# Optimization experiments

Hardware: AMD Instinct MI355X
Metric: run time of the kernel (lower is better)

Reference implementation:

```python
import jax, jax.numpy as jnp
import numpy as np

N = 100000       # nodes
E = 1600000      # edges (avg degree 16)
F_IN = 128       # ogb_feature_dim
HID = 128        # hidden_dim
C = 40           # num_class


def setup_inputs() -> dict:
    key = jax.random.key(0)
    ks = jax.random.split(key, 6)
    w = lambda k, sh: jax.random.normal(k, sh, jnp.float32) * 0.05
    return {
        "x": jax.random.normal(ks[0], (N, F_IN), jnp.float32),
        "edge_index": jax.random.randint(ks[1], (2, E), 0, N),
        "W1": w(ks[2], (F_IN, HID)), "b1": jnp.zeros((HID,), jnp.float32),
        "W2": w(ks[3], (HID, HID)), "b2": jnp.zeros((HID,), jnp.float32),
        "W3": w(ks[4], (HID, C)),  "b3": jnp.zeros((C,), jnp.float32),
    }


def _gcn_conv(h, row, col, deg_inv_sqrt, W, b, num_nodes):
    # PyG GCNConv: x' = D^{-1/2} (A + I) D^{-1/2} (x W) + b
    h = h @ W                                   # [N, out]
    norm = deg_inv_sqrt[row] * deg_inv_sqrt[col]  # [E+N]
    msg = h[row] * norm[:, None]                # gather + scale (irregular)
    out = jax.ops.segment_sum(msg, col, num_segments=num_nodes)  # scatter-add
    return out + b


def reference(x, edge_index, W1, b1, W2, b2, W3, b3):
    num_nodes = x.shape[0]
    loops = jnp.arange(num_nodes, dtype=edge_index.dtype)
    row = jnp.concatenate([edge_index[0], loops])  # add self-loops
    col = jnp.concatenate([edge_index[1], loops])
    deg = jax.ops.segment_sum(jnp.ones_like(col, jnp.float32), col,
                              num_segments=num_nodes)
    deg_inv_sqrt = jax.lax.rsqrt(jnp.maximum(deg, 1e-12))  # deg>=1 (self-loops)

    h = _gcn_conv(x, row, col, deg_inv_sqrt, W1, b1, num_nodes)
    h = jax.nn.relu(h)  # dropout is identity in eval mode
    h = _gcn_conv(h, row, col, deg_inv_sqrt, W2, b2, num_nodes)
    h = jax.nn.relu(h)
    h = _gcn_conv(h, row, col, deg_inv_sqrt, W3, b3, num_nodes)
    return jax.nn.log_softmax(h, axis=1)
```

## Files before the change

kernel.cpp:

```cpp
#include <hip/hip_runtime.h>
#include <hip/hip_bf16.h>
#include <math.h>


__device__ inline float bfu(unsigned short s) {
    return __uint_as_float((unsigned)s << 16);
}
__device__ inline float bf16lo(unsigned u) { return __uint_as_float(u << 16); }
__device__ inline float bf16hi(unsigned u) { return __uint_as_float(u & 0xFFFF0000u); }
__device__ inline unsigned packbf2(float a, float b) {
    __hip_bfloat16 x = __float2bfloat16(a), y = __float2bfloat16(b);
    unsigned short ux = *(unsigned short*)&x, uy = *(unsigned short*)&y;
    return (unsigned)ux | ((unsigned)uy << 16);
}
__device__ inline unsigned short bf1(float a) {
    __hip_bfloat16 x = __float2bfloat16(a);
    return *(unsigned short*)&x;
}

__global__ __launch_bounds__(256) void k_bhist(const int* __restrict__ col, int E,
                                               int NB, int* __restrict__ bhist) {
    __shared__ int h[512];
    for (int j = threadIdx.x; j < 512; j += 256) h[j] = 0;
    __syncthreads();
    int chunk = (E + gridDim.x - 1) / gridDim.x;
    int lo = blockIdx.x * chunk;
    int hi = min(lo + chunk, E);
    for (int i = lo + threadIdx.x; i < hi; i += 256)
        atomicAdd(&h[col[i] >> 8], 1);
    __syncthreads();
    for (int j = threadIdx.x; j < NB; j += 256) {
        int v = h[j];
        if (v) atomicAdd(&bhist[j], v);
    }
}

__global__ __launch_bounds__(512) void k_bscan(const int* __restrict__ bhist,
                                               int NB, int E,
                                               int* __restrict__ bbase,
                                               int* __restrict__ bcur) {
    __shared__ int sm[512];
    int t = threadIdx.x;
    int v = (t < NB) ? bhist[t] : 0;
    sm[t] = v;
    __syncthreads();
    for (int off = 1; off < 512; off <<= 1) {
        int u = (t >= off) ? sm[t - off] : 0;
        __syncthreads();
        sm[t] += u;
        __syncthreads();
    }
    if (t < NB) {
        int ex = sm[t] - v;
        bbase[t] = ex;
        bcur[t] = ex;
    }
    if (t == 0) bbase[NB] = E;
}

__global__ __launch_bounds__(256) void k_bin2(const int* __restrict__ row,
                                              const int* __restrict__ col, int E,
                                              int* __restrict__ bcur,
                                              unsigned* __restrict__ binned) {
    __shared__ int h[512];
    __shared__ int base[512];
    int t = threadIdx.x;
    for (int j = t; j < 512; j += 256) h[j] = 0;
    __syncthreads();
    int chunk = (E + gridDim.x - 1) / gridDim.x;
    int lo = blockIdx.x * chunk;
    int hi = min(lo + chunk, E);
    for (int i = lo + t; i < hi; i += 256)
        atomicAdd(&h[col[i] >> 8], 1);
    __syncthreads();
    for (int j = t; j < 512; j += 256) {
        int c = h[j];
        base[j] = c ? atomicAdd(&bcur[j], c) : 0;
    }
    __syncthreads();
    for (int i = lo + t; i < hi; i += 256) {
        int r = row[i], c = col[i];
        int p = atomicAdd(&base[c >> 8], 1);
        binned[p] = (unsigned)r | ((unsigned)(c & 255) << 24);
    }
}

__global__ __launch_bounds__(256) void k_cntB(const unsigned* __restrict__ binned,
                                              const int* __restrict__ bbase,
                                              int N, int* __restrict__ cnt) {
    int b = blockIdx.x, t = threadIdx.x;
    __shared__ int sc[256];
    sc[t] = 0;
    __syncthreads();
    int lo = bbase[b], hi = bbase[b + 1];
    for (int i = lo + t; i < hi; i += 256)
        atomicAdd(&sc[binned[i] >> 24], 1);
    __syncthreads();
    int node = b * 256 + t;
    if (node < N) cnt[node] = sc[t];
}

__global__ __launch_bounds__(256) void k_bsum(const int* __restrict__ cnt, int N,
                                              int* __restrict__ bsum) {
    int t = threadIdx.x;
    int base = blockIdx.x * 1024 + t * 4;
    int s = 0;
    if (base + 3 < N) {
        int4 v = *(const int4*)(cnt + base);
        s = v.x + v.y + v.z + v.w;
    } else {
        for (int j = 0; j < 4; ++j)
            if (base + j < N) s += cnt[base + j];
    }
#pragma unroll
    for (int off = 32; off; off >>= 1) s += __shfl_xor(s, off);
    __shared__ int ws[4];
    int lane = t & 63, w = t >> 6;
    if (lane == 0) ws[w] = s;
    __syncthreads();
    if (t == 0) bsum[blockIdx.x] = ws[0] + ws[1] + ws[2] + ws[3];
}

__global__ __launch_bounds__(128) void k_sbsum(int* __restrict__ bsum, int B) {
    __shared__ int sm[128];
    int t = threadIdx.x;
    int v = (t < B) ? bsum[t] : 0;
    sm[t] = v;
    __syncthreads();
    for (int off = 1; off < 128; off <<= 1) {
        int u = (t >= off) ? sm[t - off] : 0;
        __syncthreads();
        sm[t] += u;
        __syncthreads();
    }
    if (t < B) bsum[t] = sm[t] - v;
}

__global__ __launch_bounds__(256) void k_wptr(const int* __restrict__ cnt,
                                              const int* __restrict__ bsum, int N,
                                              int* __restrict__ ptr,
                                              float* __restrict__ dis) {
    int t = threadIdx.x;
    int base = blockIdx.x * 1024 + t * 4;
    int c[4];
    int s = 0;
    if (base + 3 < N) {
        int4 v = *(const int4*)(cnt + base);
        c[0] = v.x; c[1] = v.y; c[2] = v.z; c[3] = v.w;
        s = v.x + v.y + v.z + v.w;
    } else {
#pragma unroll
        for (int j = 0; j < 4; ++j) {
            c[j] = (base + j < N) ? cnt[base + j] : 0;
            s += c[j];
        }
    }
    int lane = t & 63, w = t >> 6;
    int incl = s;
#pragma unroll
    for (int off = 1; off < 64; off <<= 1) {
        int u = __shfl_up(incl, off);
        if (lane >= off) incl += u;
    }
    __shared__ int wsum[4];
    if (lane == 63) wsum[w] = incl;
    __syncthreads();
    int run = bsum[blockIdx.x] + (incl - s);
    for (int j = 0; j < w; ++j) run += wsum[j];
#pragma unroll
    for (int j = 0; j < 4; ++j) {
        int i = base + j;
        if (i < N) {
            ptr[i] = run;
            dis[i] = rsqrtf((float)(c[j] + 1));
            run += c[j];
        }
    }
}

__global__ __launch_bounds__(256) void k_fill2(const unsigned* __restrict__ binned,
                                               const int* __restrict__ bbase,
                                               const int* __restrict__ ptr, int N,
                                               int* __restrict__ esrc) {
    int b = blockIdx.x, t = threadIdx.x;
    __shared__ int lc[256];
    int node = b * 256 + t;
    lc[t] = (node < N) ? ptr[node] : 0;
    __syncthreads();
    int lo = bbase[b], hi = bbase[b + 1];
    for (int i = lo + t; i < hi; i += 256) {
        unsigned e = binned[i];
        int p = atomicAdd(&lc[e >> 24], 1);
        esrc[p] = (int)(e & 0xFFFFFFu);
    }
}

__global__ __launch_bounds__(256) void k_gemm128_f32(const float* __restrict__ X,
                                                     const float* __restrict__ W,
                                                     unsigned short* __restrict__ Y,
                                                     int M) {
    __shared__ float wsm[64 * 128];
    __shared__ float xs[64 * 68];
    int t = threadIdx.x;
    int row0 = blockIdx.x * 64;
    int cg = t & 15, rg = t >> 4;
    float acc[4][8];
#pragma unroll
    for (int a = 0; a < 4; ++a)
#pragma unroll
        for (int b = 0; b < 8; ++b) acc[a][b] = 0.f;

    for (int kp = 0; kp < 2; ++kp) {
        const float4* W4 = (const float4*)W;
        float4* wd = (float4*)wsm;
#pragma unroll
        for (int i = 0; i < 8; ++i) {
            int idx = t + i * 256;
            wd[idx] = W4[kp * 2048 + idx];
        }
        const float4* X4 = (const float4*)X;
#pragma unroll
        for (int i = 0; i < 4; ++i) {
            int idx = t + i * 256;
            int r = idx >> 4, c4 = idx & 15;
            float4 v = {0.f, 0.f, 0.f, 0.f};
            if (row0 + r < M) v = X4[(size_t)(row0 + r) * 32 + kp * 16 + c4];
            float* dst = &xs[r * 68 + c4 * 4];
            dst[0] = v.x; dst[1] = v.y; dst[2] = v.z; dst[3] = v.w;
        }
        __syncthreads();
#pragma unroll 4
        for (int k = 0; k < 64; ++k) {
            float a0 = xs[(rg * 4 + 0) * 68 + k];
            float a1 = xs[(rg * 4 + 1) * 68 + k];
            float a2 = xs[(rg * 4 + 2) * 68 + k];
            float a3 = xs[(rg * 4 + 3) * 68 + k];
            const float* wr = &wsm[k * 128 + cg * 8];
            float4 w0 = *(const float4*)wr;
            float4 w1 = *(const float4*)(wr + 4);
            float wv[8] = {w0.x, w0.y, w0.z, w0.w, w1.x, w1.y, w1.z, w1.w};
#pragma unroll
            for (int b = 0; b < 8; ++b) {
                acc[0][b] = fmaf(a0, wv[b], acc[0][b]);
                acc[1][b] = fmaf(a1, wv[b], acc[1][b]);
                acc[2][b] = fmaf(a2, wv[b], acc[2][b]);
                acc[3][b] = fmaf(a3, wv[b], acc[3][b]);
            }
        }
        __syncthreads();
    }
#pragma unroll
    for (int a = 0; a < 4; ++a) {
        int r = row0 + rg * 4 + a;
        if (r < M) {
            uint4 o;
            o.x = packbf2(acc[a][0], acc[a][1]);
            o.y = packbf2(acc[a][2], acc[a][3]);
            o.z = packbf2(acc[a][4], acc[a][5]);
            o.w = packbf2(acc[a][6], acc[a][7]);
            *(uint4*)&Y[(size_t)r * 128 + cg * 8] = o;
        }
    }
}

__global__ __launch_bounds__(256) void k_gemm128_bf16(const unsigned short* __restrict__ X,
                                                      const float* __restrict__ W,
                                                      unsigned short* __restrict__ Y,
                                                      int M) {
    __shared__ float wsm[64 * 128];
    __shared__ float xs[64 * 68];
    int t = threadIdx.x;
    int row0 = blockIdx.x * 64;
    int cg = t & 15, rg = t >> 4;
    float acc[4][8];
#pragma unroll
    for (int a = 0; a < 4; ++a)
#pragma unroll
        for (int b = 0; b < 8; ++b) acc[a][b] = 0.f;

    for (int kp = 0; kp < 2; ++kp) {
        const float4* W4 = (const float4*)W;
        float4* wd = (float4*)wsm;
#pragma unroll
        for (int i = 0; i < 8; ++i) {
            int idx = t + i * 256;
            wd[idx] = W4[kp * 2048 + idx];
        }
        const ushort4* X4 = (const ushort4*)X;
#pragma unroll
        for (int i = 0; i < 4; ++i) {
            int idx = t + i * 256;
            int r = idx >> 4, c4 = idx & 15;
            float v0 = 0.f, v1 = 0.f, v2 = 0.f, v3 = 0.f;
            if (row0 + r < M) {
                ushort4 v = X4[(size_t)(row0 + r) * 32 + kp * 16 + c4];
                v0 = bfu(v.x); v1 = bfu(v.y); v2 = bfu(v.z); v3 = bfu(v.w);
            }
            float* dst = &xs[r * 68 + c4 * 4];
            dst[0] = v0; dst[1] = v1; dst[2] = v2; dst[3] = v3;
        }
        __syncthreads();
#pragma unroll 4
        for (int k = 0; k < 64; ++k) {
            float a0 = xs[(rg * 4 + 0) * 68 + k];
            float a1 = xs[(rg * 4 + 1) * 68 + k];
            float a2 = xs[(rg * 4 + 2) * 68 + k];
            float a3 = xs[(rg * 4 + 3) * 68 + k];
            const float* wr = &wsm[k * 128 + cg * 8];
            float4 w0 = *(const float4*)wr;
            float4 w1 = *(const float4*)(wr + 4);
            float wv[8] = {w0.x, w0.y, w0.z, w0.w, w1.x, w1.y, w1.z, w1.w};
#pragma unroll
            for (int b = 0; b < 8; ++b) {
                acc[0][b] = fmaf(a0, wv[b], acc[0][b]);
                acc[1][b] = fmaf(a1, wv[b], acc[1][b]);
                acc[2][b] = fmaf(a2, wv[b], acc[2][b]);
                acc[3][b] = fmaf(a3, wv[b], acc[3][b]);
            }
        }
        __syncthreads();
    }
#pragma unroll
    for (int a = 0; a < 4; ++a) {
        int r = row0 + rg * 4 + a;
        if (r < M) {
            uint4 o;
            o.x = packbf2(acc[a][0], acc[a][1]);
            o.y = packbf2(acc[a][2], acc[a][3]);
            o.z = packbf2(acc[a][4], acc[a][5]);
            o.w = packbf2(acc[a][6], acc[a][7]);
            *(uint4*)&Y[(size_t)r * 128 + cg * 8] = o;
        }
    }
}

__global__ __launch_bounds__(320) void k_gemm40(const unsigned short* __restrict__ X,
                                                const float* __restrict__ W,
                                                float* __restrict__ Y, int M) {
    __shared__ float wsm[128 * 40];
    __shared__ float xs[64 * 133];
    int t = threadIdx.x;
    int row0 = blockIdx.x * 64;
    for (int idx = t; idx < 128 * 40; idx += 320) wsm[idx] = W[idx];
    const ushort4* X4 = (const ushort4*)X;
    for (int idx = t; idx < 2048; idx += 320) {
        int r = idx >> 5, c4 = idx & 31;
        float v0 = 0.f, v1 = 0.f, v2 = 0.f, v3 = 0.f;
        if (row0 + r < M) {
            ushort4 v = X4[(size_t)(row0 + r) * 32 + c4];
            v0 = bfu(v.x); v1 = bfu(v.y); v2 = bfu(v.z); v3 = bfu(v.w);
        }
        float* dst = &xs[r * 133 + c4 * 4];
        dst[0] = v0; dst[1] = v1; dst[2] = v2; dst[3] = v3;
    }
    __syncthreads();
    int lane = t & 63, cg = t >> 6;
    float acc[8];
#pragma unroll
    for (int b = 0; b < 8; ++b) acc[b] = 0.f;
#pragma unroll 4
    for (int k = 0; k < 128; ++k) {
        float a = xs[lane * 133 + k];
        const float* wr = &wsm[k * 40 + cg * 8];
        float4 w0 = *(const float4*)wr;
        float4 w1 = *(const float4*)(wr + 4);
        acc[0] = fmaf(a, w0.x, acc[0]); acc[1] = fmaf(a, w0.y, acc[1]);
        acc[2] = fmaf(a, w0.z, acc[2]); acc[3] = fmaf(a, w0.w, acc[3]);
        acc[4] = fmaf(a, w1.x, acc[4]); acc[5] = fmaf(a, w1.y, acc[5]);
        acc[6] = fmaf(a, w1.z, acc[6]); acc[7] = fmaf(a, w1.w, acc[7]);
    }
    int r = row0 + lane;
    if (r < M) {
        float4* dst = (float4*)&Y[(size_t)r * 40 + cg * 8];
        float4 o0 = {acc[0], acc[1], acc[2], acc[3]};
        float4 o1 = {acc[4], acc[5], acc[6], acc[7]};
        dst[0] = o0;
        dst[1] = o1;
    }
}

__global__ __launch_bounds__(256) void k_agg128(const unsigned short* __restrict__ h,
                                                const float* __restrict__ dis,
                                                const int* __restrict__ ptr,
                                                const int* __restrict__ cnt,
                                                const int* __restrict__ esrc,
                                                const float* __restrict__ bias,
                                                unsigned short* __restrict__ out,
                                                int relu, int N) {
    int node = blockIdx.x * 4 + (threadIdx.x >> 6);
    if (node >= N) return;
    int lane = threadIdx.x & 63;
    float di = dis[node];
    const unsigned* h32 = (const unsigned*)h;
    unsigned su = h32[(size_t)node * 64 + lane];
    float w = di * di;
    float ax = bf16lo(su) * w, ay = bf16hi(su) * w;
    int start = ptr[node], c = cnt[node];
    for (int base = 0; base < c; base += 64) {
        int m = min(64, c - base);
        int e = 0;
        float dsl = 0.f;
        if (lane < m) {
            e = esrc[start + base + lane];
            dsl = dis[e];
        }
        int j = 0;
        for (; j + 2 <= m; j += 2) {
            int sA = __shfl(e, j), sB = __shfl(e, j + 1);
            float scA = __shfl(dsl, j) * di;
            float scB = __shfl(dsl, j + 1) * di;
            unsigned uA = h32[(size_t)sA * 64 + lane];
            unsigned uB = h32[(size_t)sB * 64 + lane];
            ax = fmaf(bf16lo(uA), scA, ax); ay = fmaf(bf16hi(uA), scA, ay);
            ax = fmaf(bf16lo(uB), scB, ax); ay = fmaf(bf16hi(uB), scB, ay);
        }
        if (j < m) {
            int sA = __shfl(e, j);
            float scA = __shfl(dsl, j) * di;
            unsigned uA = h32[(size_t)sA * 64 + lane];
            ax = fmaf(bf16lo(uA), scA, ax); ay = fmaf(bf16hi(uA), scA, ay);
        }
    }
    float2 b = ((const float2*)bias)[lane];
    ax += b.x; ay += b.y;
    if (relu) { ax = fmaxf(ax, 0.f); ay = fmaxf(ay, 0.f); }
    ((unsigned*)out)[(size_t)node * 64 + lane] = packbf2(ax, ay);
}

__global__ __launch_bounds__(256) void k_agg40(const float* __restrict__ h,
                                               const float* __restrict__ dis,
                                               const int* __restrict__ ptr,
                                               const int* __restrict__ cnt,
                                               const int* __restrict__ esrc,
                                               const float* __restrict__ bias,
                                               float* __restrict__ out, int N) {
    int node = blockIdx.x * 4 + (threadIdx.x >> 6);
    if (node >= N) return;
    int lane = threadIdx.x & 63;
    float di = dis[node];
    float acc = 0.f;
    if (lane < 40) acc = h[(size_t)node * 40 + lane] * di * di;
    int start = ptr[node], c = cnt[node];
    for (int base = 0; base < c; base += 64) {
        int m = min(64, c - base);
        int e = 0;
        float dsl = 0.f;
        if (lane < m) {
            e = esrc[start + base + lane];
            dsl = dis[e];
        }
        for (int j = 0; j < m; ++j) {
            int s = __shfl(e, j);
            float sc = __shfl(dsl, j) * di;
            if (lane < 40) acc = fmaf(h[(size_t)s * 40 + lane], sc, acc);
        }
    }
    if (lane < 40) out[(size_t)node * 40 + lane] = acc + bias[lane];
}

__global__ __launch_bounds__(256) void k_lsm(const float* __restrict__ in,
                                             float* __restrict__ out, int N) {
    int rowi = blockIdx.x * 4 + (threadIdx.x >> 6);
    if (rowi >= N) return;
    int lane = threadIdx.x & 63;
    float v = (lane < 40) ? in[(size_t)rowi * 40 + lane] : -INFINITY;
    float m = v;
#pragma unroll
    for (int o = 32; o; o >>= 1) m = fmaxf(m, __shfl_xor(m, o));
    float ex = (lane < 40) ? expf(v - m) : 0.f;
    float s = ex;
#pragma unroll
    for (int o = 32; o; o >>= 1) s += __shfl_xor(s, o);
    if (lane < 40) out[(size_t)rowi * 40 + lane] = v - m - logf(s);
}

extern "C" void kernel_launch(void* const* d_in, const int* in_sizes, int n_in,
                              void* d_out, int out_size, void* d_ws, size_t ws_size,
                              hipStream_t stream) {
    const float* x  = (const float*)d_in[0];
    const int*   ei = (const int*)d_in[1];
    const float* W1 = (const float*)d_in[2];
    const float* b1 = (const float*)d_in[3];
    const float* W2 = (const float*)d_in[4];
    const float* b2 = (const float*)d_in[5];
    const float* W3 = (const float*)d_in[6];
    const float* b3 = (const float*)d_in[7];
    int N = in_sizes[0] / 128;
    int E = in_sizes[1] / 2;
    const int* row = ei;
    const int* col = ei + E;
    int NB = (N + 255) >> 8;

    char* ws = (char*)d_ws;
    size_t off = 0;
    auto alloc = [&](size_t bytes) {
        void* p = ws + off;
        off += (bytes + 255) & ~(size_t)255;
        return p;
    };
    unsigned short* hA = (unsigned short*)alloc((size_t)N * 128 * 2);
    unsigned short* hB = (unsigned short*)alloc((size_t)N * 128 * 2);
    float* t3    = (float*)alloc((size_t)N * 40 * 4);
    float* t3b   = (float*)alloc((size_t)N * 40 * 4);
    int*   esrc  = (int*)alloc((size_t)E * 4);
    int*   cptr  = (int*)alloc((size_t)N * 4);
    int*   cnt   = (int*)alloc((size_t)N * 4);
    float* dis   = (float*)alloc((size_t)N * 4);
    int*   bsum  = (int*)alloc(256 * 4);
    int*   bhist = (int*)alloc(512 * 4);
    int*   bbase = (int*)alloc(513 * 4);
    int*   bcur  = (int*)alloc(512 * 4);
    unsigned* binned = (unsigned*)hB;

    hipMemsetAsync(bhist, 0, 512 * 4, stream);
    k_bhist<<<256, 256, 0, stream>>>(col, E, NB, bhist);
    k_bscan<<<1, 512, 0, stream>>>(bhist, NB, E, bbase, bcur);
    k_bin2<<<256, 256, 0, stream>>>(row, col, E, bcur, binned);
    k_cntB<<<NB, 256, 0, stream>>>(binned, bbase, N, cnt);
    int B = (N + 1023) / 1024;
    k_bsum<<<B, 256, 0, stream>>>(cnt, N, bsum);
    k_sbsum<<<1, 128, 0, stream>>>(bsum, B);
    k_wptr<<<B, 256, 0, stream>>>(cnt, bsum, N, cptr, dis);
    k_fill2<<<NB, 256, 0, stream>>>(binned, bbase, cptr, N, esrc);

    int gb = (N + 63) / 64;
    int ab = (N + 3) / 4;
    k_gemm128_f32<<<gb, 256, 0, stream>>>(x, W1, hA, N);
    k_agg128<<<ab, 256, 0, stream>>>(hA, dis, cptr, cnt, esrc, b1, hB, 1, N);
    k_gemm128_bf16<<<gb, 256, 0, stream>>>(hB, W2, hA, N);
    k_agg128<<<ab, 256, 0, stream>>>(hA, dis, cptr, cnt, esrc, b2, hB, 1, N);
    k_gemm40<<<gb, 320, 0, stream>>>(hB, W3, t3, N);
    k_agg40<<<ab, 256, 0, stream>>>(t3, dis, cptr, cnt, esrc, b3, t3b, N);
    k_lsm<<<ab, 256, 0, stream>>>(t3b, (float*)d_out, N);
}
```

Baseline: 577.5 us.

## Reorder last GCN layer to aggregate before GEMM and fuse bias with log-softmax

After: 546.9 us. -5.3%, faster.

```diff
diff --git a/kernel.cpp b/kernel.cpp
--- a/kernel.cpp
+++ b/kernel.cpp
@@ -12,10 +12,6 @@
     __hip_bfloat16 x = __float2bfloat16(a), y = __float2bfloat16(b);
     unsigned short ux = *(unsigned short*)&x, uy = *(unsigned short*)&y;
     return (unsigned)ux | ((unsigned)uy << 16);
-}
-__device__ inline unsigned short bf1(float a) {
-    __hip_bfloat16 x = __float2bfloat16(a);
-    return *(unsigned short*)&x;
 }
 
 __global__ __launch_bounds__(256) void k_bhist(const int* __restrict__ col, int E,
@@ -334,11 +330,14 @@
     }
 }
 
-__global__ __launch_bounds__(320) void k_gemm40(const unsigned short* __restrict__ X,
-                                                const float* __restrict__ W,
-                                                float* __restrict__ Y, int M) {
+__global__ __launch_bounds__(320) void k_gemm40f(const unsigned short* __restrict__ X,
+                                                 const float* __restrict__ W,
+                                                 const float* __restrict__ bias,
+                                                 float* __restrict__ out, int M) {
     __shared__ float wsm[128 * 40];
     __shared__ float xs[64 * 133];
+    __shared__ float osm[64 * 40];
+    __shared__ float rm[64], rls[64];
     int t = threadIdx.x;
     int row0 = blockIdx.x * 64;
     for (int idx = t; idx < 128 * 40; idx += 320) wsm[idx] = W[idx];
@@ -369,11 +368,28 @@
         acc[4] = fmaf(a, w1.x, acc[4]); acc[5] = fmaf(a, w1.y, acc[5]);
         acc[6] = fmaf(a, w1.z, acc[6]); acc[7] = fmaf(a, w1.w, acc[7]);
     }
+#pragma unroll
+    for (int b = 0; b < 8; ++b) {
+        acc[b] += bias[cg * 8 + b];
+        osm[lane * 40 + cg * 8 + b] = acc[b];
+    }
+    __syncthreads();
+    if (t < 64) {
+        const float* rowv = &osm[t * 40];
+        float m = rowv[0];
+        for (int k = 1; k < 40; ++k) m = fmaxf(m, rowv[k]);
+        float s = 0.f;
+        for (int k = 0; k < 40; ++k) s += expf(rowv[k] - m);
+        rm[t] = m;
+        rls[t] = logf(s);
+    }
+    __syncthreads();
     int r = row0 + lane;
     if (r < M) {
-        float4* dst = (float4*)&Y[(size_t)r * 40 + cg * 8];
-        float4 o0 = {acc[0], acc[1], acc[2], acc[3]};
-        float4 o1 = {acc[4], acc[5], acc[6], acc[7]};
+        float sub = rm[lane] + rls[lane];
+        float4* dst = (float4*)&out[(size_t)r * 40 + cg * 8];
+        float4 o0 = {acc[0] - sub, acc[1] - sub, acc[2] - sub, acc[3] - sub};
+        float4 o1 = {acc[4] - sub, acc[5] - sub, acc[6] - sub, acc[7] - sub};
         dst[0] = o0;
         dst[1] = o1;
     }
@@ -421,57 +437,12 @@
             ax = fmaf(bf16lo(uA), scA, ax); ay = fmaf(bf16hi(uA), scA, ay);
         }
     }
-    float2 b = ((const float2*)bias)[lane];
-    ax += b.x; ay += b.y;
+    if (bias) {
+        float2 b = ((const float2*)bias)[lane];
+        ax += b.x; ay += b.y;
+    }
     if (relu) { ax = fmaxf(ax, 0.f); ay = fmaxf(ay, 0.f); }
     ((unsigned*)out)[(size_t)node * 64 + lane] = packbf2(ax, ay);
-}
-
-__global__ __launch_bounds__(256) void k_agg40(const float* __restrict__ h,
-                                               const float* __restrict__ dis,
-                                               const int* __restrict__ ptr,
-                                               const int* __restrict__ cnt,
-                                               const int* __restrict__ esrc,
-                                               const float* __restrict__ bias,
-                                               float* __restrict__ out, int N) {
-    int node = blockIdx.x * 4 + (threadIdx.x >> 6);
-    if (node >= N) return;
-    int lane = threadIdx.x & 63;
-    float di = dis[node];
-    float acc = 0.f;
-    if (lane < 40) acc = h[(size_t)node * 40 + lane] * di * di;
-    int start = ptr[node], c = cnt[node];
-    for (int base = 0; base < c; base += 64) {
-        int m = min(64, c - base);
-        int e = 0;
-        float dsl = 0.f;
-        if (lane < m) {
-            e = esrc[start + base + lane];
-            dsl = dis[e];
-        }
-        for (int j = 0; j < m; ++j) {
-            int s = __shfl(e, j);
-            float sc = __shfl(dsl, j) * di;
-            if (lane < 40) acc = fmaf(h[(size_t)s * 40 + lane], sc, acc);
-        }
-    }
-    if (lane < 40) out[(size_t)node * 40 + lane] = acc + bias[lane];
-}
-
-__global__ __launch_bounds__(256) void k_lsm(const float* __restrict__ in,
-                                             float* __restrict__ out, int N) {
-    int rowi = blockIdx.x * 4 + (threadIdx.x >> 6);
-    if (rowi >= N) return;
-    int lane = threadIdx.x & 63;
-    float v = (lane < 40) ? in[(size_t)rowi * 40 + lane] : -INFINITY;
-    float m = v;
-#pragma unroll
-    for (int o = 32; o; o >>= 1) m = fmaxf(m, __shfl_xor(m, o));
-    float ex = (lane < 40) ? expf(v - m) : 0.f;
-    float s = ex;
-#pragma unroll
-    for (int o = 32; o; o >>= 1) s += __shfl_xor(s, o);
-    if (lane < 40) out[(size_t)rowi * 40 + lane] = v - m - logf(s);
 }
 
 extern "C" void kernel_launch(void* const* d_in, const int* in_sizes, int n_in,
@@ -500,8 +471,6 @@
     };
     unsigned short* hA = (unsigned short*)alloc((size_t)N * 128 * 2);
     unsigned short* hB = (unsigned short*)alloc((size_t)N * 128 * 2);
-    float* t3    = (float*)alloc((size_t)N * 40 * 4);
-    float* t3b   = (float*)alloc((size_t)N * 40 * 4);
     int*   esrc  = (int*)alloc((size_t)E * 4);
     int*   cptr  = (int*)alloc((size_t)N * 4);
     int*   cnt   = (int*)alloc((size_t)N * 4);
@@ -529,7 +498,6 @@
     k_agg128<<<ab, 256, 0, stream>>>(hA, dis, cptr, cnt, esrc, b1, hB, 1, N);
     k_gemm128_bf16<<<gb, 256, 0, stream>>>(hB, W2, hA, N);
     k_agg128<<<ab, 256, 0, stream>>>(hA, dis, cptr, cnt, esrc, b2, hB, 1, N);
-    k_gemm40<<<gb, 320, 0, stream>>>(hB, W3, t3, N);
-    k_agg40<<<ab, 256, 0, stream>>>(t3, dis, cptr, cnt, esrc, b3, t3b, N);
-    k_lsm<<<ab, 256, 0, stream>>>(t3b, (float*)d_out, N);
-}
+    k_agg128<<<ab, 256, 0, stream>>>(hB, dis, cptr, cnt, esrc, nullptr, hA, 0, N);
+    k_gemm40f<<<gb, 320, 0, stream>>>(hA, W3, b3, (float*)d_out, N);
+}
```
